# Kernel optimization log

Measured on AMD Instinct MI355X. Metric: run time of the kernel, lower is better.

## Reference

```python
import jax, jax.numpy as jnp
import numpy as np

N_SRC = 131072
N_DST = 65536
N_EDGES = 524288
D_IN = 128
D_OUT = 128


def setup_inputs() -> dict:
    key = jax.random.key(0)
    k1, k2, k3, k4, k5 = jax.random.split(key, 5)
    feat = jax.random.normal(k1, (N_SRC, D_IN), dtype=jnp.float32)
    # xavier_uniform-ish scale for the two projections
    lim = float(np.sqrt(6.0 / (D_IN + D_OUT))) * np.sqrt(2.0)
    W_self = jax.random.uniform(k2, (D_IN, D_OUT), jnp.float32, -lim, lim)
    W_neigh = jax.random.uniform(k3, (D_IN, D_OUT), jnp.float32, -lim, lim)
    b_self = jnp.zeros((D_OUT,), jnp.float32)
    b_neigh = jnp.zeros((D_OUT,), jnp.float32)
    src_idx = jax.random.randint(k4, (N_EDGES,), 0, N_SRC, dtype=jnp.int32)
    dst_idx = jnp.sort(jax.random.randint(k5, (N_EDGES,), 0, N_DST, dtype=jnp.int32))
    return {
        "feat": feat,
        "W_self": W_self,
        "b_self": b_self,
        "W_neigh": W_neigh,
        "b_neigh": b_neigh,
        "src_idx": src_idx,
        "dst_idx": dst_idx,
        "num_row": N_DST,
    }


def reference(feat, W_self, b_self, W_neigh, b_neigh, src_idx, dst_idx, num_row):
    # h_self: destination-node features (first num_row rows)
    h_self = feat[:num_row, :]                              # [num_row, D_IN]
    # csrmm: mean aggregation of source neighbor features per destination row
    gathered = feat[src_idx]                                # [E, D_IN]
    neigh_sum = jax.ops.segment_sum(gathered, dst_idx, num_segments=num_row)
    deg = jax.ops.segment_sum(jnp.ones_like(dst_idx, dtype=feat.dtype), dst_idx,
                              num_segments=num_row)
    h_neigh = neigh_sum / jnp.maximum(deg, 1.0)[:, None]    # [num_row, D_IN]
    # dual linear projections
    rst = (h_self @ W_self + b_self) + (h_neigh @ W_neigh + b_neigh)
    return rst
```

## Files before the change

kernel.cpp:

```cpp
#include <hip/hip_runtime.h>
#include <hip/hip_bf16.h>

#define N_SRC   131072
#define N_DST   65536
#define D       128

typedef __bf16 bf16x8 __attribute__((ext_vector_type(8)));
typedef __bf16 bf16x4 __attribute__((ext_vector_type(4)));
typedef float  f32x4  __attribute__((ext_vector_type(4)));

__global__ __launch_bounds__(256) void boundaries_kernel(
    const int* __restrict__ dst, int n_edges, int* __restrict__ row_start)
{
    const int e = blockIdx.x * 256 + threadIdx.x;
    if (e >= n_edges) return;
    const int d    = dst[e];
    const int prev = (e == 0) ? -1 : dst[e - 1];
    for (int r = prev + 1; r <= d; ++r) row_start[r] = e;
    if (e == n_edges - 1) {
        for (int r = d + 1; r <= N_DST; ++r) row_start[r] = n_edges;
    }
}

__global__ __launch_bounds__(128) void prep_w_kernel(
    const float* __restrict__ W_self, const float* __restrict__ W_neigh,
    __bf16* __restrict__ Wt_self, __bf16* __restrict__ Wt_neigh)
{
    const int k = blockIdx.x;
    const int n = threadIdx.x;
    Wt_self [n * D + k] = (__bf16)W_self [k * D + n];
    Wt_neigh[n * D + k] = (__bf16)W_neigh[k * D + n];
}

__global__ __launch_bounds__(256) void neigh_kernel(
    const float* __restrict__ feat,
    const int*   __restrict__ src,
    const int*   __restrict__ row_start,
    __bf16*      __restrict__ h_neigh)
{
    const int g    = threadIdx.x >> 5;
    const int lane = threadIdx.x & 31;
    const int row  = blockIdx.x * 8 + g;
    const int s0   = row_start[row];
    const int s1   = row_start[row + 1];

    float ax = 0.f, ay = 0.f, az = 0.f, aw = 0.f;
    const int co = lane * 4;

    int e = s0;
    for (; e + 4 <= s1; e += 4) {
        const int ia = src[e + 0];
        const int ib = src[e + 1];
        const int ic = src[e + 2];
        const int id = src[e + 3];
        const float4 va = *(const float4*)&feat[(size_t)ia * D + co];
        const float4 vb = *(const float4*)&feat[(size_t)ib * D + co];
        const float4 vc = *(const float4*)&feat[(size_t)ic * D + co];
        const float4 vd = *(const float4*)&feat[(size_t)id * D + co];
        ax += (va.x + vb.x) + (vc.x + vd.x);
        ay += (va.y + vb.y) + (vc.y + vd.y);
        az += (va.z + vb.z) + (vc.z + vd.z);
        aw += (va.w + vb.w) + (vc.w + vd.w);
    }
    for (; e < s1; ++e) {
        const int s = src[e];
        const float4 v = *(const float4*)&feat[(size_t)s * D + co];
        ax += v.x; ay += v.y; az += v.z; aw += v.w;
    }

    const float inv = 1.0f / fmaxf((float)(s1 - s0), 1.0f);
    bf16x4 o;
    o[0] = (__bf16)(ax * inv);
    o[1] = (__bf16)(ay * inv);
    o[2] = (__bf16)(az * inv);
    o[3] = (__bf16)(aw * inv);
    *(bf16x4*)&h_neigh[(size_t)row * D + co] = o;
}

#define MREP 2

__global__ __launch_bounds__(256) void gemm_kernel(
    const float*  __restrict__ feat,
    const __bf16* __restrict__ h_neigh,
    const __bf16* __restrict__ Wt_self,
    const __bf16* __restrict__ Wt_neigh,
    const float*  __restrict__ b_self,
    const float*  __restrict__ b_neigh,
    float*        __restrict__ out)
{
    const int t    = threadIdx.x;
    const int w    = t >> 6;
    const int l    = t & 63;
    const int m16  = l & 15;
    const int quad = l >> 4;
    const int kb   = quad * 8;
    const int rowbase = blockIdx.x * (64 * MREP) + w * (16 * MREP);

    f32x4 acc[MREP][8];
    #pragma unroll
    for (int rp = 0; rp < MREP; ++rp)
        #pragma unroll
        for (int nb = 0; nb < 8; ++nb)
            acc[rp][nb] = (f32x4){0.f, 0.f, 0.f, 0.f};

    #pragma unroll
    for (int ks = 0; ks < 4; ++ks) {
        bf16x8 afrag[MREP];
        #pragma unroll
        for (int rp = 0; rp < MREP; ++rp) {
            const float* ap = &feat[(size_t)(rowbase + rp * 16 + m16) * D + ks * 32 + kb];
            const float4 a0 = *(const float4*)ap;
            const float4 a1 = *(const float4*)(ap + 4);
            afrag[rp][0] = (__bf16)a0.x; afrag[rp][1] = (__bf16)a0.y;
            afrag[rp][2] = (__bf16)a0.z; afrag[rp][3] = (__bf16)a0.w;
            afrag[rp][4] = (__bf16)a1.x; afrag[rp][5] = (__bf16)a1.y;
            afrag[rp][6] = (__bf16)a1.z; afrag[rp][7] = (__bf16)a1.w;
        }
        #pragma unroll
        for (int nb = 0; nb < 8; ++nb) {
            const bf16x8 bfrag = *(const bf16x8*)&Wt_self[(size_t)(nb * 16 + m16) * D + ks * 32 + kb];
            #pragma unroll
            for (int rp = 0; rp < MREP; ++rp)
                acc[rp][nb] = __builtin_amdgcn_mfma_f32_16x16x32_bf16(
                    afrag[rp], bfrag, acc[rp][nb], 0, 0, 0);
        }
    }

    #pragma unroll
    for (int ks = 0; ks < 4; ++ks) {
        bf16x8 afrag[MREP];
        #pragma unroll
        for (int rp = 0; rp < MREP; ++rp)
            afrag[rp] = *(const bf16x8*)&h_neigh[(size_t)(rowbase + rp * 16 + m16) * D + ks * 32 + kb];
        #pragma unroll
        for (int nb = 0; nb < 8; ++nb) {
            const bf16x8 bfrag = *(const bf16x8*)&Wt_neigh[(size_t)(nb * 16 + m16) * D + ks * 32 + kb];
            #pragma unroll
            for (int rp = 0; rp < MREP; ++rp)
                acc[rp][nb] = __builtin_amdgcn_mfma_f32_16x16x32_bf16(
                    afrag[rp], bfrag, acc[rp][nb], 0, 0, 0);
        }
    }

    #pragma unroll
    for (int nb = 0; nb < 8; ++nb) {
        const int col = nb * 16 + m16;
        const float bias = b_self[col] + b_neigh[col];
        #pragma unroll
        for (int rp = 0; rp < MREP; ++rp) {
            const int orow0 = rowbase + rp * 16 + quad * 4;
            #pragma unroll
            for (int r = 0; r < 4; ++r)
                out[(size_t)(orow0 + r) * D + col] = acc[rp][nb][r] + bias;
        }
    }
}

extern "C" void kernel_launch(void* const* d_in, const int* in_sizes, int n_in,
                              void* d_out, int out_size, void* d_ws, size_t ws_size,
                              hipStream_t stream)
{
    const float* feat    = (const float*)d_in[0];
    const float* W_self  = (const float*)d_in[1];
    const float* b_self  = (const float*)d_in[2];
    const float* W_neigh = (const float*)d_in[3];
    const float* b_neigh = (const float*)d_in[4];
    const int*   src_idx = (const int*)d_in[5];
    const int*   dst_idx = (const int*)d_in[6];
    const int n_edges = in_sizes[5];

    char* ws = (char*)d_ws;
    __bf16* h_neigh  = (__bf16*)ws;
    int*    row_start = (int*)(ws + (size_t)N_DST * D * 2);
    __bf16* Wt_self  = (__bf16*)(ws + (size_t)N_DST * D * 2 + 262400);
    __bf16* Wt_neigh = Wt_self + D * D;

    boundaries_kernel<<<(n_edges + 255) / 256, 256, 0, stream>>>(dst_idx, n_edges, row_start);
    prep_w_kernel<<<D, D, 0, stream>>>(W_self, W_neigh, Wt_self, Wt_neigh);
    neigh_kernel<<<N_DST / 8, 256, 0, stream>>>(feat, src_idx, row_start, h_neigh);
    gemm_kernel<<<N_DST / (64 * MREP), 256, 0, stream>>>(
        feat, h_neigh, Wt_self, Wt_neigh, b_self, b_neigh, (float*)d_out);
}
```

Before: 170.7 us.

## Pre-convert features to bf16 once and gather bf16 rows in aggregation

A new prep kernel converts the whole fp32 feature matrix to bf16 in one pass. The same launch also computes the row boundaries and transposes the weights, merging three small launches into one. The neighbour-mean kernel now gathers 256-byte bf16 rows with 16 lanes per row, and the GEMM reads bf16 self features directly. The aim is to halve the bytes moved by the random gather and the GEMM A-operand reads. In exchange there is an extra full read and write of the feature matrix, and neighbour sums are built from bf16-rounded inputs, so accuracy drops slightly.

```diff
diff --git a/kernel.cpp b/kernel.cpp
--- a/kernel.cpp
+++ b/kernel.cpp
@@ -6,81 +6,95 @@
 #define D       128
 
 typedef __bf16 bf16x8 __attribute__((ext_vector_type(8)));
-typedef __bf16 bf16x4 __attribute__((ext_vector_type(4)));
 typedef float  f32x4  __attribute__((ext_vector_type(4)));
 
-__global__ __launch_bounds__(256) void boundaries_kernel(
-    const int* __restrict__ dst, int n_edges, int* __restrict__ row_start)
+#define CONV_BLOCKS 8192
+#define W_BLOCKS    64
+
+__global__ __launch_bounds__(256) void prep_kernel(
+    const float* __restrict__ feat,
+    const int*   __restrict__ dst, int n_edges, int n_bnd_blocks,
+    const float* __restrict__ W_self, const float* __restrict__ W_neigh,
+    __bf16* __restrict__ feat_bf,
+    int*    __restrict__ row_start,
+    __bf16* __restrict__ Wt_self, __bf16* __restrict__ Wt_neigh)
 {
-    const int e = blockIdx.x * 256 + threadIdx.x;
-    if (e >= n_edges) return;
-    const int d    = dst[e];
-    const int prev = (e == 0) ? -1 : dst[e - 1];
-    for (int r = prev + 1; r <= d; ++r) row_start[r] = e;
-    if (e == n_edges - 1) {
-        for (int r = d + 1; r <= N_DST; ++r) row_start[r] = n_edges;
+    const int b = blockIdx.x;
+    const int t = threadIdx.x;
+
+    if (b < CONV_BLOCKS) {
+        const size_t i0 = ((size_t)b * 256 + t) * 8;
+        const float4 a0 = *(const float4*)&feat[i0];
+        const float4 a1 = *(const float4*)&feat[i0 + 4];
+        bf16x8 o;
+        o[0] = (__bf16)a0.x; o[1] = (__bf16)a0.y; o[2] = (__bf16)a0.z; o[3] = (__bf16)a0.w;
+        o[4] = (__bf16)a1.x; o[5] = (__bf16)a1.y; o[6] = (__bf16)a1.z; o[7] = (__bf16)a1.w;
+        *(bf16x8*)&feat_bf[i0] = o;
+    } else if (b < CONV_BLOCKS + n_bnd_blocks) {
+        const int e = (b - CONV_BLOCKS) * 256 + t;
+        if (e < n_edges) {
+            const int d    = dst[e];
+            const int prev = (e == 0) ? -1 : dst[e - 1];
+            for (int r = prev + 1; r <= d; ++r) row_start[r] = e;
+            if (e == n_edges - 1)
+                for (int r = d + 1; r <= N_DST; ++r) row_start[r] = n_edges;
+        }
+    } else {
+        const int wb  = b - CONV_BLOCKS - n_bnd_blocks;
+        const int idx = wb * 256 + t;
+        const int k = idx >> 7, n = idx & 127;
+        Wt_self [n * D + k] = (__bf16)W_self [k * D + n];
+        Wt_neigh[n * D + k] = (__bf16)W_neigh[k * D + n];
     }
 }
 
-__global__ __launch_bounds__(128) void prep_w_kernel(
-    const float* __restrict__ W_self, const float* __restrict__ W_neigh,
-    __bf16* __restrict__ Wt_self, __bf16* __restrict__ Wt_neigh)
+__global__ __launch_bounds__(256) void neigh_kernel(
+    const __bf16* __restrict__ feat_bf,
+    const int*    __restrict__ src,
+    const int*    __restrict__ row_start,
+    __bf16*       __restrict__ h_neigh)
 {
-    const int k = blockIdx.x;
-    const int n = threadIdx.x;
-    Wt_self [n * D + k] = (__bf16)W_self [k * D + n];
-    Wt_neigh[n * D + k] = (__bf16)W_neigh[k * D + n];
-}
-
-__global__ __launch_bounds__(256) void neigh_kernel(
-    const float* __restrict__ feat,
-    const int*   __restrict__ src,
-    const int*   __restrict__ row_start,
-    __bf16*      __restrict__ h_neigh)
-{
-    const int g    = threadIdx.x >> 5;
-    const int lane = threadIdx.x & 31;
-    const int row  = blockIdx.x * 8 + g;
+    const int g    = threadIdx.x >> 4;
+    const int lane = threadIdx.x & 15;
+    const int row  = blockIdx.x * 16 + g;
     const int s0   = row_start[row];
     const int s1   = row_start[row + 1];
+    const int co   = lane * 8;
 
-    float ax = 0.f, ay = 0.f, az = 0.f, aw = 0.f;
-    const int co = lane * 4;
+    float acc[8] = {0.f, 0.f, 0.f, 0.f, 0.f, 0.f, 0.f, 0.f};
 
     int e = s0;
     for (; e + 4 <= s1; e += 4) {
-        const int ia = src[e + 0];
-        const int ib = src[e + 1];
-        const int ic = src[e + 2];
-        const int id = src[e + 3];
-        const float4 va = *(const float4*)&feat[(size_t)ia * D + co];
-        const float4 vb = *(const float4*)&feat[(size_t)ib * D + co];
-        const float4 vc = *(const float4*)&feat[(size_t)ic * D + co];
-        const float4 vd = *(const float4*)&feat[(size_t)id * D + co];
-        ax += (va.x + vb.x) + (vc.x + vd.x);
-        ay += (va.y + vb.y) + (vc.y + vd.y);
-        az += (va.z + vb.z) + (vc.z + vd.z);
-        aw += (va.w + vb.w) + (vc.w + vd.w);
+        const int sa = src[e + 0];
+        const int sb = src[e + 1];
+        const int sc = src[e + 2];
+        const int sd = src[e + 3];
+        const bf16x8 va = *(const bf16x8*)&feat_bf[(size_t)sa * D + co];
+        const bf16x8 vb = *(const bf16x8*)&feat_bf[(size_t)sb * D + co];
+        const bf16x8 vc = *(const bf16x8*)&feat_bf[(size_t)sc * D + co];
+        const bf16x8 vd = *(const bf16x8*)&feat_bf[(size_t)sd * D + co];
+        #pragma unroll
+        for (int j = 0; j < 8; ++j)
+            acc[j] += ((float)va[j] + (float)vb[j]) + ((float)vc[j] + (float)vd[j]);
     }
     for (; e < s1; ++e) {
         const int s = src[e];
-        const float4 v = *(const float4*)&feat[(size_t)s * D + co];
-        ax += v.x; ay += v.y; az += v.z; aw += v.w;
+        const bf16x8 v = *(const bf16x8*)&feat_bf[(size_t)s * D + co];
+        #pragma unroll
+        for (int j = 0; j < 8; ++j) acc[j] += (float)v[j];
     }
 
     const float inv = 1.0f / fmaxf((float)(s1 - s0), 1.0f);
-    bf16x4 o;
-    o[0] = (__bf16)(ax * inv);
-    o[1] = (__bf16)(ay * inv);
-    o[2] = (__bf16)(az * inv);
-    o[3] = (__bf16)(aw * inv);
-    *(bf16x4*)&h_neigh[(size_t)row * D + co] = o;
+    bf16x8 o;
+    #pragma unroll
+    for (int j = 0; j < 8; ++j) o[j] = (__bf16)(acc[j] * inv);
+    *(bf16x8*)&h_neigh[(size_t)row * D + co] = o;
 }
 
 #define MREP 2
 
 __global__ __launch_bounds__(256) void gemm_kernel(
-    const float*  __restrict__ feat,
+    const __bf16* __restrict__ feat_bf,
     const __bf16* __restrict__ h_neigh,
     const __bf16* __restrict__ Wt_self,
     const __bf16* __restrict__ Wt_neigh,
@@ -103,48 +117,33 @@
         for (int nb = 0; nb < 8; ++nb)
             acc[rp][nb] = (f32x4){0.f, 0.f, 0.f, 0.f};
 
+    const __bf16* __restrict__ Aptr[2] = {feat_bf, h_neigh};
+    const __bf16* __restrict__ Wptr[2] = {Wt_self, Wt_neigh};
+
     #pragma unroll
-    for (int ks = 0; ks < 4; ++ks) {
-        bf16x8 afrag[MREP];
+    for (int p = 0; p < 2; ++p) {
+        const __bf16* __restrict__ A = Aptr[p];
+        const __bf16* __restrict__ W = Wptr[p];
         #pragma unroll
-        for (int rp = 0; rp < MREP; ++rp) {
-            const float* ap = &feat[(size_t)(rowbase + rp * 16 + m16) * D + ks * 32 + kb];
-            const float4 a0 = *(const float4*)ap;
-            const float4 a1 = *(const float4*)(ap + 4);
-            afrag[rp][0] = (__bf16)a0.x; afrag[rp][1] = (__bf16)a0.y;
-            afrag[rp][2] = (__bf16)a0.z; afrag[rp][3] = (__bf16)a0.w;
-            afrag[rp][4] = (__bf16)a1.x; afrag[rp][5] = (__bf16)a1.y;
-            afrag[rp][6] = (__bf16)a1.z; afrag[rp][7] = (__bf16)a1.w;
-        }
-        #pragma unroll
-        for (int nb = 0; nb < 8; ++nb) {
-            const bf16x8 bfrag = *(const bf16x8*)&Wt_self[(size_t)(nb * 16 + m16) * D + ks * 32 + kb];
+        for (int ks = 0; ks < 4; ++ks) {
+            bf16x8 afrag[MREP];
             #pragma unroll
             for (int rp = 0; rp < MREP; ++rp)
-                acc[rp][nb] = __builtin_amdgcn_mfma_f32_16x16x32_bf16(
-                    afrag[rp], bfrag, acc[rp][nb], 0, 0, 0);
-        }
-    }
-
-    #pragma unroll
-    for (int ks = 0; ks < 4; ++ks) {
-        bf16x8 afrag[MREP];
-        #pragma unroll
-        for (int rp = 0; rp < MREP; ++rp)
-            afrag[rp] = *(const bf16x8*)&h_neigh[(size_t)(rowbase + rp * 16 + m16) * D + ks * 32 + kb];
-        #pragma unroll
-        for (int nb = 0; nb < 8; ++nb) {
-            const bf16x8 bfrag = *(const bf16x8*)&Wt_neigh[(size_t)(nb * 16 + m16) * D + ks * 32 + kb];
+                afrag[rp] = *(const bf16x8*)&A[(size_t)(rowbase + rp * 16 + m16) * D + ks * 32 + kb];
             #pragma unroll
-            for (int rp = 0; rp < MREP; ++rp)
-                acc[rp][nb] = __builtin_amdgcn_mfma_f32_16x16x32_bf16(
-                    afrag[rp], bfrag, acc[rp][nb], 0, 0, 0);
+            for (int nb = 0; nb < 8; ++nb) {
+                const bf16x8 bfrag = *(const bf16x8*)&W[(size_t)(nb * 16 + m16) * D + ks * 32 + kb];
+                #pragma unroll
+                for (int rp = 0; rp < MREP; ++rp)
+                    acc[rp][nb] = __builtin_amdgcn_mfma_f32_16x16x32_bf16(
+                        afrag[rp], bfrag, acc[rp][nb], 0, 0, 0);
+            }
         }
     }
 
     #pragma unroll
     for (int nb = 0; nb < 8; ++nb) {
-        const int col = nb * 16 + m16;
+        const int col  = nb * 16 + m16;
         const float bias = b_self[col] + b_neigh[col];
         #pragma unroll
         for (int rp = 0; rp < MREP; ++rp) {
@@ -170,14 +169,19 @@
     const int n_edges = in_sizes[5];
 
     char* ws = (char*)d_ws;
-    __bf16* h_neigh  = (__bf16*)ws;
-    int*    row_start = (int*)(ws + (size_t)N_DST * D * 2);
-    __bf16* Wt_self  = (__bf16*)(ws + (size_t)N_DST * D * 2 + 262400);
+    __bf16* feat_bf  = (__bf16*)ws;
+    __bf16* h_neigh  = feat_bf + (size_t)N_SRC * D;
+    int*    row_start = (int*)(h_neigh + (size_t)N_DST * D);
+    __bf16* Wt_self  = (__bf16*)(row_start + N_DST + 16);
     __bf16* Wt_neigh = Wt_self + D * D;
 
-    boundaries_kernel<<<(n_edges + 255) / 256, 256, 0, stream>>>(dst_idx, n_edges, row_start);
-    prep_w_kernel<<<D, D, 0, stream>>>(W_self, W_neigh, Wt_self, Wt_neigh);
-    neigh_kernel<<<N_DST / 8, 256, 0, stream>>>(feat, src_idx, row_start, h_neigh);
+    const int n_bnd = (n_edges + 255) / 256;
+    prep_kernel<<<CONV_BLOCKS + n_bnd + W_BLOCKS, 256, 0, stream>>>(
+        feat, dst_idx, n_edges, n_bnd, W_self, W_neigh,
+        feat_bf, row_start, Wt_self, Wt_neigh);
+
+    neigh_kernel<<<N_DST / 16, 256, 0, stream>>>(feat_bf, src_idx, row_start, h_neigh);
+
     gemm_kernel<<<N_DST / (64 * MREP), 256, 0, stream>>>(
-        feat, h_neigh, Wt_self, Wt_neigh, b_self, b_neigh, (float*)d_out);
+        feat_bf, h_neigh, Wt_self, Wt_neigh, b_self, b_neigh, (float*)d_out);
 }
```

Result: faster. 166.8 us (-2.3%).
